# Kernel tuning notes

Hardware: AMD Instinct MI355X
Metric: run time of the kernel (lower is better)

## Reference

```python
import jax, jax.numpy as jnp
import numpy as np

B, T, D, H = 2, 2048, 1024, 16
HD = D // H  # 64


def _rotary_tables(t, hd):
    # standard RoPE cos/sin tables, shape [T, hd]
    inv_freq = 1.0 / (10000.0 ** (jnp.arange(0, hd, 2, dtype=jnp.float32) / hd))
    freqs = jnp.arange(t, dtype=jnp.float32)[:, None] * inv_freq[None, :]  # [T, hd/2]
    emb = jnp.concatenate([freqs, freqs], axis=-1)  # [T, hd]
    return jnp.cos(emb), jnp.sin(emb)


def setup_inputs() -> dict:
    key = jax.random.key(0)
    kx, kq, kk, kv, kp = jax.random.split(key, 5)
    x = jax.random.normal(kx, (B, T, D), dtype=jnp.float32)
    cos_t, sin_t = _rotary_tables(T, HD)
    cos = jnp.broadcast_to(cos_t[None], (B, T, HD)).astype(jnp.float32)
    sin = jnp.broadcast_to(sin_t[None], (B, T, HD)).astype(jnp.float32)
    scale = 0.02
    Wq = jax.random.normal(kq, (D, D), dtype=jnp.float32) * scale
    Wk = jax.random.normal(kk, (D, D), dtype=jnp.float32) * scale
    Wv = jax.random.normal(kv, (D, D), dtype=jnp.float32) * scale
    Wp = jax.random.normal(kp, (D, D), dtype=jnp.float32) * scale
    return {"x": x, "cos": cos, "sin": sin, "Wq": Wq, "Wk": Wk, "Wv": Wv, "Wp": Wp}


def _rotate_half(x):
    x1, x2 = jnp.split(x, 2, axis=-1)
    return jnp.concatenate([-x2, x1], axis=-1)


def reference(x, cos, sin, Wq, Wk, Wv, Wp):
    b, t, d = x.shape
    h, hd = H, HD
    # torch Linear: y = x @ W.T
    q = jnp.einsum('btd,ed->bte', x, Wq).reshape(b, t, h, hd)
    k = jnp.einsum('btd,ed->bte', x, Wk).reshape(b, t, h, hd)
    v = jnp.einsum('btd,ed->bte', x, Wv).reshape(b, t, h, hd)
    # RoPE, cos/sin [B,T,hd] -> broadcast over heads (unsqueeze_dim=2)
    c = cos[:, :, None, :]
    s = sin[:, :, None, :]
    q = q * c + _rotate_half(q) * s
    k = k * c + _rotate_half(k) * s
    # causal attention, softmax scale = 1/sqrt(head_dim) (flash_attn default)
    scale = 1.0 / np.sqrt(hd).astype(np.float32)
    scores = jnp.einsum('bqhd,bkhd->bhqk', q, k) * scale  # [B,H,T,T]
    mask = jnp.tril(jnp.ones((t, t), dtype=bool))
    scores = jnp.where(mask[None, None], scores, jnp.finfo(scores.dtype).min)
    probs = jax.nn.softmax(scores, axis=-1)
    out = jnp.einsum('bhqk,bkhd->bqhd', probs, v).reshape(b, t, d)
    return jnp.einsum('btd,ed->bte', out, Wp)
```

## Files before the change

kernel.cpp:

```cpp
#include <hip/hip_runtime.h>
#include <hip/hip_bf16.h>

typedef __attribute__((ext_vector_type(8))) short bf16x8s;
typedef __attribute__((ext_vector_type(4))) float f32x4;
typedef __attribute__((ext_vector_type(16))) float f32x16;
typedef __attribute__((ext_vector_type(4))) __bf16 bf16x4;
typedef __attribute__((ext_vector_type(8))) __bf16 bf16x8;

typedef const __attribute__((address_space(1))) void gvoid_t;
typedef __attribute__((address_space(3))) void lvoid_t;

constexpr int Bc = 2, Tc = 2048, Dc = 1024, Hc = 16, HDc = 64;
constexpr int Mc = Bc * Tc;

__global__ void cvt_all(const float* __restrict__ x,
                        const float* __restrict__ wq, const float* __restrict__ wk,
                        const float* __restrict__ wv, const float* __restrict__ wp,
                        __bf16* __restrict__ xb, __bf16* __restrict__ wb) {
  const int bid = blockIdx.x;
  const float* src;
  __bf16* dst;
  int i;
  if (bid < 4096) {
    src = x; dst = xb; i = (bid * 256 + threadIdx.x) * 4;
  } else {
    const int r = bid - 4096;
    const int w = r >> 10;
    src = (w == 0) ? wq : (w == 1) ? wk : (w == 2) ? wv : wp;
    dst = wb + (size_t)w * (Dc * Dc);
    i = ((r & 1023) * 256 + threadIdx.x) * 4;
  }
  float4 v = *(const float4*)(src + i);
  bf16x4 o;
  o[0] = (__bf16)v.x; o[1] = (__bf16)v.y; o[2] = (__bf16)v.z; o[3] = (__bf16)v.w;
  *(bf16x4*)(dst + i) = o;
}

__launch_bounds__(256, 2)
__global__ void gemm_qkv(const __bf16* __restrict__ A,
                         const __bf16* __restrict__ W,
                         __bf16* __restrict__ outb,
                         __bf16* __restrict__ vtout,
                         const float* __restrict__ cbt,
                         const float* __restrict__ sbt) {
  __shared__ __bf16 smem[2][128 * 64];
  __bf16* Alds = smem[0];
  __bf16* Blds = smem[1];
  const int tid = threadIdx.x;
  const int lane = tid & 63, wid = tid >> 6;
  const int wr = wid >> 1, wc = wid & 1;
  const int lr = lane & 15, lg = lane >> 4;
  const int lid = blockIdx.x + (int)gridDim.x * blockIdx.y;
  const int xcd = lid & 7, g = lid >> 3;
  const int brow = (xcd * 4 + (g & 3)) * 128;
  const int bcol = (g >> 2) * 128;
  const __bf16* Wm = W + (size_t)blockIdx.z * (Dc * Dc);

  f32x4 acc[4][4] = {};

  const char* Ag = (const char*)(A + (size_t)brow * Dc);
  const char* Bg = (const char*)(Wm + (size_t)bcol * Dc);
  const int r0 = tid >> 3;
  const int cb = (tid & 7) * 16;

  for (int k0 = 0; k0 < Dc; k0 += 64) {
#pragma unroll
    for (int i = 0; i < 4; ++i) {
      const int r = i * 32 + r0;
      const int ldsoff = (i * 256 + wid * 64) * 16;
      __builtin_amdgcn_global_load_lds(
          (gvoid_t*)(Ag + (size_t)r * (Dc * 2) + k0 * 2 + cb),
          (lvoid_t*)((char*)Alds + ldsoff), 16, 0, 0);
      __builtin_amdgcn_global_load_lds(
          (gvoid_t*)(Bg + (size_t)r * (Dc * 2) + k0 * 2 + cb),
          (lvoid_t*)((char*)Blds + ldsoff), 16, 0, 0);
    }
    __syncthreads();
#pragma unroll
    for (int kk = 0; kk < 2; ++kk) {
      const int col = kk * 32 + lg * 8;
      bf16x8s af[4], bfv[4];
#pragma unroll
      for (int m = 0; m < 4; ++m)
        af[m] = *(const bf16x8s*)(Alds + (wr * 64 + m * 16 + lr) * 64 + col);
#pragma unroll
      for (int n = 0; n < 4; ++n)
        bfv[n] = *(const bf16x8s*)(Blds + (wc * 64 + n * 16 + lr) * 64 + col);
#pragma unroll
      for (int m = 0; m < 4; ++m)
#pragma unroll
        for (int n = 0; n < 4; ++n)
          acc[m][n] = __builtin_amdgcn_mfma_f32_16x16x32_bf16(af[m], bfv[n], acc[m][n], 0, 0, 0);
    }
    __syncthreads();
  }

  const int z = blockIdx.z;
  if (z == 2) {
    const int bb = brow >> 11, t0b = brow & (Tc - 1);
    __bf16* tile_t = smem[0];
#pragma unroll
    for (int h2 = 0; h2 < 2; ++h2) {
      __syncthreads();
      if (wc == h2) {
#pragma unroll
        for (int n = 0; n < 4; ++n) {
#pragma unroll
          for (int m = 0; m < 4; ++m) {
            bf16x4 pb;
#pragma unroll
            for (int j = 0; j < 4; ++j) pb[j] = (__bf16)acc[m][n][j];
            *(bf16x4*)(tile_t + (n * 16 + lr) * 136 + wr * 64 + m * 16 + lg * 4) = pb;
          }
        }
      }
      __syncthreads();
#pragma unroll
      for (int pass = 0; pass < 4; ++pass) {
        const int r = pass * 16 + (tid >> 4);
        const int c8 = (tid & 15) * 8;
        bf16x8 vvv = *(const bf16x8*)(tile_t + r * 136 + c8);
        const int gn = bcol + h2 * 64 + r;
        const int h = gn >> 6, hd = gn & 63;
        *(bf16x8*)(vtout + (((size_t)bb * Hc + h) * HDc + hd) * Tc + t0b + c8) = vvv;
      }
    }
    return;
  }

  {
    const float scl = (z == 0) ? 0.18033688011112042f : 1.0f;
#pragma unroll
    for (int m = 0; m < 4; ++m) {
#pragma unroll
      for (int j = 0; j < 4; ++j) {
        const int gm = brow + wr * 64 + m * 16 + lg * 4 + j;
        const float* cbase = cbt + (size_t)gm * HDc;
        const float* sbase = sbt + (size_t)gm * HDc;
#pragma unroll
        for (int n = 0; n < 2; ++n) {
          const int i = n * 16 + lr;
          const float c0 = cbase[i], s0 = sbase[i];
          const float c1 = cbase[i + 32], s1 = sbase[i + 32];
          const float v0 = acc[m][n][j], v1 = acc[m][n + 2][j];
          acc[m][n][j]     = (v0 * c0 - v1 * s0) * scl;
          acc[m][n + 2][j] = (v1 * c1 + v0 * s1) * scl;
        }
      }
    }
    __bf16* dst = outb + (size_t)z * ((size_t)Mc * Dc);
#pragma unroll
    for (int m = 0; m < 4; ++m) {
#pragma unroll
      for (int j = 0; j < 4; ++j) {
        const int gm = brow + wr * 64 + m * 16 + lg * 4 + j;
        const int bb = gm >> 11, t = gm & (Tc - 1);
#pragma unroll
        for (int n = 0; n < 4; ++n) {
          const int gn = bcol + wc * 64 + n * 16 + lr;
          const int h = gn >> 6, hd = gn & 63;
          dst[(((size_t)bb * Hc + h) * Tc + t) * HDc + hd] = (__bf16)acc[m][n][j];
        }
      }
    }
  }
}

__launch_bounds__(256, 2)
__global__ void gemm_proj(const __bf16* __restrict__ A, const __bf16* __restrict__ W,
                          float* __restrict__ outf) {
  __shared__ __bf16 Alds[128 * 64];
  __shared__ __bf16 Blds[64 * 64];
  const int tid = threadIdx.x;
  const int lane = tid & 63, wid = tid >> 6;
  const int lr = lane & 15, lg = lane >> 4;
  const int lid = blockIdx.x + (int)gridDim.x * blockIdx.y;
  const int xcd = lid & 7, g = lid >> 3;
  const int brow = (xcd * 4 + (g & 3)) * 128;
  const int bcol = (g >> 2) * 64;
  f32x4 acc[2][4] = {};
  const char* Ag = (const char*)(A + (size_t)brow * Dc);
  const char* Bg = (const char*)(W + (size_t)bcol * Dc);
  const int r0 = tid >> 3;
  const int cb = (tid & 7) * 16;
  for (int k0 = 0; k0 < Dc; k0 += 64) {
#pragma unroll
    for (int i = 0; i < 4; ++i) {
      const int r = i * 32 + r0;
      const int ldsoff = (i * 256 + wid * 64) * 16;
      __builtin_amdgcn_global_load_lds(
          (gvoid_t*)(Ag + (size_t)r * (Dc * 2) + k0 * 2 + cb),
          (lvoid_t*)((char*)Alds + ldsoff), 16, 0, 0);
    }
#pragma unroll
    for (int i = 0; i < 2; ++i) {
      const int r = i * 32 + r0;
      const int ldsoff = (i * 256 + wid * 64) * 16;
      __builtin_amdgcn_global_load_lds(
          (gvoid_t*)(Bg + (size_t)r * (Dc * 2) + k0 * 2 + cb),
          (lvoid_t*)((char*)Blds + ldsoff), 16, 0, 0);
    }
    __syncthreads();
#pragma unroll
    for (int kk = 0; kk < 2; ++kk) {
      const int col = kk * 32 + lg * 8;
      bf16x8s af[2], bfv[4];
#pragma unroll
      for (int m = 0; m < 2; ++m)
        af[m] = *(const bf16x8s*)(Alds + (wid * 32 + m * 16 + lr) * 64 + col);
#pragma unroll
      for (int n = 0; n < 4; ++n)
        bfv[n] = *(const bf16x8s*)(Blds + (n * 16 + lr) * 64 + col);
#pragma unroll
      for (int m = 0; m < 2; ++m)
#pragma unroll
        for (int n = 0; n < 4; ++n)
          acc[m][n] = __builtin_amdgcn_mfma_f32_16x16x32_bf16(af[m], bfv[n], acc[m][n], 0, 0, 0);
    }
    __syncthreads();
  }
#pragma unroll
  for (int m = 0; m < 2; ++m)
#pragma unroll
    for (int j = 0; j < 4; ++j) {
      const int gm = brow + wid * 32 + m * 16 + lg * 4 + j;
#pragma unroll
      for (int n = 0; n < 4; ++n) {
        const int gn = bcol + n * 16 + lr;
        outf[(size_t)gm * Dc + gn] = acc[m][n][j];
      }
    }
}

__launch_bounds__(128, 2)
__global__ void attn_kernel(const __bf16* __restrict__ Q, const __bf16* __restrict__ K,
                            const __bf16* __restrict__ Vt, __bf16* __restrict__ O) {
  __shared__ __bf16 Klds[2][64 * 64];
  __shared__ __bf16 Vlds[2][64 * 64];
  __shared__ __bf16 Plds[2][32 * 64];
  const int f = blockIdx.x;
  const int xcd = f & 7, g = f >> 3;
  const int bh = xcd * 4 + (g & 3);
  const int qblk = 31 - (g >> 2);
  const int tid = threadIdx.x;
  const int lane = tid & 63, wid = tid >> 6;
  const int q31 = lane & 31, hh = lane >> 5;
  const int k3 = q31 & 7;
  const __bf16* Qp = Q + (size_t)bh * Tc * HDc;
  const char* Kb = (const char*)(K + (size_t)bh * Tc * HDc);
  const char* Vb = (const char*)(Vt + (size_t)bh * HDc * Tc);

  const int units = qblk + 1;

  const int srow = wid * 32 + (lane >> 3);
  const int sxor = ((lane & 7) ^ ((lane >> 3) & 7)) << 4;
  const char* vsrc = Vb + (size_t)srow * (Tc * 2) + sxor;

  const int q0w = qblk * 64 + wid * 32;
  bf16x8s qf[4];
#pragma unroll
  for (int ks = 0; ks < 4; ++ks)
    qf[ks] = *(const bf16x8s*)(Qp + (q0w + q31) * HDc + ks * 16 + hh * 8);

  char* Pw = (char*)&Plds[wid][0];
  const int b = bh >> 4, h = bh & 15;

  f32x16 acc0 = {}, acc1 = {};
  float lsum = 0.f;

#define STAGE(IT, BUF)                                                                   \
  do {                                                                                   \
    _Pragma("unroll")                                                                    \
    for (int i_ = 0; i_ < 4; ++i_) {                                                     \
      __builtin_amdgcn_global_load_lds(                                                  \
          (gvoid_t*)(Kb + (size_t)((IT) * 64 + srow + i_ * 8) * 128 + sxor),             \
          (lvoid_t*)((char*)Klds[BUF] + wid * 4096 + i_ * 1024), 16, 0, 0);              \
      __builtin_amdgcn_global_load_lds(                                                  \
          (gvoid_t*)(vsrc + (size_t)i_ * 8 * (Tc * 2) + (IT) * 128),                     \
          (lvoid_t*)((char*)Vlds[BUF] + wid * 4096 + i_ * 1024), 16, 0, 0);              \
    }                                                                                    \
  } while (0)

  STAGE(0, 0);
  asm volatile("s_waitcnt vmcnt(0)" ::: "memory");
  __builtin_amdgcn_sched_barrier(0);
  __builtin_amdgcn_s_barrier();
  __builtin_amdgcn_sched_barrier(0);

  for (int u = 0; u < units; ++u) {
    if (u + 1 < units) STAGE(u + 1, (u + 1) & 1);
    __builtin_amdgcn_sched_barrier(0);

    const int kv0 = u * 64;
    const char* Kl = (const char*)Klds[u & 1];
    const char* Vl = (const char*)Vlds[u & 1];
    const bool fin = (u == units - 1);
    const int thr = q0w + q31 - kv0 - 4 * hh;

#pragma unroll
    for (int ct = 0; ct < 2; ++ct) {
      bf16x8s kf[4];
#pragma unroll
      for (int ks = 0; ks < 4; ++ks)
        kf[ks] = *(const bf16x8s*)(Kl + (ct * 32 + q31) * 128 + (((2 * ks + hh) ^ k3) << 4));
      f32x16 z = {};
      __builtin_amdgcn_s_setprio(1);
#pragma unroll
      for (int ks = 0; ks < 4; ++ks)
        z = __builtin_amdgcn_mfma_f32_32x32x16_bf16(kf[ks], qf[ks], z, 0, 0, 0);
      __builtin_amdgcn_s_setprio(0);
#pragma unroll
      for (int qd = 0; qd < 4; ++qd) {
        bf16x4 pb;
#pragma unroll
        for (int j = 0; j < 4; ++j) {
          float e = __builtin_amdgcn_exp2f(z[qd * 4 + j]);
          if (fin && (ct * 32 + qd * 8 + j > thr)) e = 0.f;
          lsum += e;
          pb[j] = (__bf16)e;
        }
        *(bf16x4*)(Pw + q31 * 128 + ((((4 * ct + qd) ^ k3) << 4) | (hh << 3))) = pb;
      }
    }

    bf16x8s pfr[4];
#pragma unroll
    for (int ks = 0; ks < 4; ++ks)
      pfr[ks] = *(const bf16x8s*)(Pw + q31 * 128 + (((2 * ks + hh) ^ k3) << 4));
    __builtin_amdgcn_s_setprio(1);
#pragma unroll
    for (int ks = 0; ks < 4; ++ks) {
      const int so = ((2 * ks + hh) ^ k3) << 4;
      const bf16x8s va0 = *(const bf16x8s*)(Vl + q31 * 128 + so);
      const bf16x8s va1 = *(const bf16x8s*)(Vl + (32 + q31) * 128 + so);
      acc0 = __builtin_amdgcn_mfma_f32_32x32x16_bf16(va0, pfr[ks], acc0, 0, 0, 0);
      acc1 = __builtin_amdgcn_mfma_f32_32x32x16_bf16(va1, pfr[ks], acc1, 0, 0, 0);
    }
    __builtin_amdgcn_s_setprio(0);

    if (u + 1 < units) {
      asm volatile("s_waitcnt vmcnt(0)" ::: "memory");
      __builtin_amdgcn_sched_barrier(0);
      __builtin_amdgcn_s_barrier();
      __builtin_amdgcn_sched_barrier(0);
    }
  }
#undef STAGE

  const float lt = lsum + __shfl_xor(lsum, 32);
  const float linv = 1.f / lt;
  const int t = q0w + q31;
  __bf16* dst = O + ((size_t)b * Tc + t) * Dc + h * HDc;
#pragma unroll
  for (int qd = 0; qd < 4; ++qd) {
    bf16x4 o0, o1;
#pragma unroll
    for (int j = 0; j < 4; ++j) {
      o0[j] = (__bf16)(acc0[qd * 4 + j] * linv);
      o1[j] = (__bf16)(acc1[qd * 4 + j] * linv);
    }
    *(bf16x4*)(dst + qd * 8 + hh * 4) = o0;
    *(bf16x4*)(dst + 32 + qd * 8 + hh * 4) = o1;
  }
}

extern "C" void kernel_launch(void* const* d_in, const int* in_sizes, int n_in,
                              void* d_out, int out_size, void* d_ws, size_t ws_size,
                              hipStream_t stream) {
  const float* x   = (const float*)d_in[0];
  const float* cbt = (const float*)d_in[1];
  const float* sbt = (const float*)d_in[2];
  const float* Wq  = (const float*)d_in[3];
  const float* Wk  = (const float*)d_in[4];
  const float* Wv  = (const float*)d_in[5];
  const float* Wp  = (const float*)d_in[6];
  float* out = (float*)d_out;
  char* ws = (char*)d_ws;
  __bf16* xb = (__bf16*)(ws);
  __bf16* wb = (__bf16*)(ws + (8u << 20));
  __bf16* qb = (__bf16*)(ws + (16u << 20));
  __bf16* vt = (__bf16*)(ws + (40u << 20));
  __bf16* ao = (__bf16*)(ws + (48u << 20));
  __bf16* kb = qb + (size_t)Mc * Dc;

  cvt_all<<<8192, 256, 0, stream>>>(x, Wq, Wk, Wv, Wp, xb, wb);
  gemm_qkv<<<dim3(8, 32, 3), 256, 0, stream>>>(xb, wb, qb, vt, cbt, sbt);
  attn_kernel<<<1024, 128, 0, stream>>>(qb, kb, vt, ao);
  gemm_proj<<<dim3(16, 32), 256, 0, stream>>>(ao, wb + 3u * (Dc * Dc), out);
}
```

Before: 110.1 us.

## Keep P in registers via permlane32 swap and reorder q-block schedule

Removes the shared-memory round trip for the softmax probability tile. P is converted to packed bf16 with v_cvt_pk_bf16_f32 and rearranged across the two half-waves with v_permlane32_swap, so the result lands directly in the B-operand layout of the PV MFMA. This frees LDS and drops a store, reload and the implied wait. It also changes block scheduling so each XCD walks heads in passes, alternating ascending and descending q-block order, to balance causal work. Correctness depends on the permlane operand mapping matching the old swizzled LDS layout.

```diff
diff --git a/kernel.cpp b/kernel.cpp
--- a/kernel.cpp
+++ b/kernel.cpp
@@ -237,11 +237,11 @@
                             const __bf16* __restrict__ Vt, __bf16* __restrict__ O) {
   __shared__ __bf16 Klds[2][64 * 64];
   __shared__ __bf16 Vlds[2][64 * 64];
-  __shared__ __bf16 Plds[2][32 * 64];
   const int f = blockIdx.x;
   const int xcd = f & 7, g = f >> 3;
-  const int bh = xcd * 4 + (g & 3);
-  const int qblk = 31 - (g >> 2);
+  const int pass = g >> 5, g5 = g & 31;
+  const int bh = xcd * 4 + pass;
+  const int qblk = (pass & 1) ? (31 - g5) : g5;
   const int tid = threadIdx.x;
   const int lane = tid & 63, wid = tid >> 6;
   const int q31 = lane & 31, hh = lane >> 5;
@@ -262,7 +262,6 @@
   for (int ks = 0; ks < 4; ++ks)
     qf[ks] = *(const bf16x8s*)(Qp + (q0w + q31) * HDc + ks * 16 + hh * 8);
 
-  char* Pw = (char*)&Plds[wid][0];
   const int b = bh >> 4, h = bh & 15;
 
   f32x16 acc0 = {}, acc1 = {};
@@ -297,6 +296,7 @@
     const bool fin = (u == units - 1);
     const int thr = q0w + q31 - kv0 - 4 * hh;
 
+    unsigned w0[8], w1[8];
 #pragma unroll
     for (int ct = 0; ct < 2; ++ct) {
       bf16x8s kf[4];
@@ -311,22 +311,32 @@
       __builtin_amdgcn_s_setprio(0);
 #pragma unroll
       for (int qd = 0; qd < 4; ++qd) {
-        bf16x4 pb;
+        float e[4];
 #pragma unroll
         for (int j = 0; j < 4; ++j) {
-          float e = __builtin_amdgcn_exp2f(z[qd * 4 + j]);
-          if (fin && (ct * 32 + qd * 8 + j > thr)) e = 0.f;
-          lsum += e;
-          pb[j] = (__bf16)e;
+          float ev = __builtin_amdgcn_exp2f(z[qd * 4 + j]);
+          if (fin && (ct * 32 + qd * 8 + j > thr)) ev = 0.f;
+          lsum += ev;
+          e[j] = ev;
         }
-        *(bf16x4*)(Pw + q31 * 128 + ((((4 * ct + qd) ^ k3) << 4) | (hh << 3))) = pb;
+        const int n = ct * 4 + qd;
+        asm("v_cvt_pk_bf16_f32 %0, %1, %2" : "=v"(w0[n]) : "v"(e[0]), "v"(e[1]));
+        asm("v_cvt_pk_bf16_f32 %0, %1, %2" : "=v"(w1[n]) : "v"(e[2]), "v"(e[3]));
       }
     }
 
     bf16x8s pfr[4];
 #pragma unroll
-    for (int ks = 0; ks < 4; ++ks)
-      pfr[ks] = *(const bf16x8s*)(Pw + q31 * 128 + (((2 * ks + hh) ^ k3) << 4));
+    for (int ks = 0; ks < 4; ++ks) {
+      unsigned a = w0[2 * ks], bb2 = w0[2 * ks + 1];
+      unsigned c = w1[2 * ks], d = w1[2 * ks + 1];
+      asm volatile("v_permlane32_swap_b32 %0, %1" : "+v"(a), "+v"(bb2));
+      asm volatile("v_permlane32_swap_b32 %0, %1" : "+v"(c), "+v"(d));
+      union { unsigned u[4]; bf16x8s v; } uu;
+      uu.u[0] = a; uu.u[1] = c; uu.u[2] = bb2; uu.u[3] = d;
+      pfr[ks] = uu.v;
+    }
+
     __builtin_amdgcn_s_setprio(1);
 #pragma unroll
     for (int ks = 0; ks < 4; ++ks) {
```

New measurement: 106.8 us. 3.0% less time.
